# Optimization experiments

Measured on AMD Instinct MI355X. Metric: run time of the kernel, lower is better.

The kernel has to match this reference:

```python
import jax, jax.numpy as jnp
import numpy as np
from jax import lax

B, T, D, H, L, V = 4, 512, 768, 768, 2, 50257


def setup_inputs() -> dict:
    key = jax.random.key(0)
    ks = jax.random.split(key, 4)
    std = 0.02
    return {
        "reps": jax.random.normal(ks[0], (B, T, D), dtype=jnp.float32),
        "W_ih": jax.random.normal(ks[1], (L, 4 * H, D), dtype=jnp.float32) * std,
        "W_hh": jax.random.normal(ks[2], (L, 4 * H, H), dtype=jnp.float32) * std,
        "b": jnp.zeros((L, 4 * H), dtype=jnp.float32),
        "head_w": jax.random.normal(ks[3], (V, H), dtype=jnp.float32) * std,
        "head_b": jnp.zeros((V,), dtype=jnp.float32),
    }


def _lstm_layer(x_tbd, W_i, W_h, bias):
    # x_tbd: (T, B, in); returns (T, B, H) hidden sequence
    b_sz = x_tbd.shape[1]
    h_dim = W_h.shape[1]
    # precompute input projections for all timesteps: (T, B, 4H)
    xg = jnp.einsum('tbd,gd->tbg', x_tbd, W_i) + bias

    def step(carry, xt_g):
        h, c = carry
        gates = xt_g + h @ W_h.T  # (B, 4H)
        i, f, g, o = jnp.split(gates, 4, axis=-1)
        i = jax.nn.sigmoid(i)
        f = jax.nn.sigmoid(f)
        g = jnp.tanh(g)
        o = jax.nn.sigmoid(o)
        c2 = f * c + i * g
        h2 = o * jnp.tanh(c2)
        return (h2, c2), h2

    h0 = jnp.zeros((b_sz, h_dim), dtype=x_tbd.dtype)
    c0 = jnp.zeros((b_sz, h_dim), dtype=x_tbd.dtype)
    _, ys = lax.scan(step, (h0, c0), xg)
    return ys


def reference(reps, W_ih, W_hh, b, head_w, head_b):
    # reps: (B, T, D) -> logits (B, T, V)
    x = jnp.swapaxes(reps, 0, 1)  # (T, B, D)
    n_layers = W_ih.shape[0]
    for l in range(n_layers):
        x = _lstm_layer(x, W_ih[l], W_hh[l], b[l])
    hidden = jnp.swapaxes(x, 0, 1)  # (B, T, H)
    return jnp.einsum('bth,vh->btv', hidden, head_w) + head_b
```

## Files before the change

kernel.cpp:

```cpp
#include <hip/hip_runtime.h>
#include <hip/hip_fp16.h>
#include <cstdint>

#define B_SZ 4
#define T_SZ 512
#define D_SZ 768
#define H_SZ 768
#define G4   3072
#define V_SZ 50257
#define V_PAD 50304
#define M_SZ 2048
#define FUSE_WGS 192

using half8 = __attribute__((ext_vector_type(8))) _Float16;
using f32x4 = __attribute__((ext_vector_type(4))) float;
typedef unsigned long long ull;


__global__ void conv_A0(const float* __restrict__ reps, _Float16* __restrict__ A0) {
  int idx = blockIdx.x * blockDim.x + threadIdx.x;
  const int total = M_SZ * D_SZ;
  for (; idx < total; idx += gridDim.x * blockDim.x) {
    int k = idx % D_SZ, m = idx / D_SZ;
    int t = m >> 2, b = m & 3;
    A0[idx] = (_Float16)reps[(b * T_SZ + t) * D_SZ + k];
  }
}

__global__ void conv_cast(const float* __restrict__ src, _Float16* __restrict__ dst, int n) {
  int idx = blockIdx.x * blockDim.x + threadIdx.x;
  for (; idx < n; idx += gridDim.x * blockDim.x) dst[idx] = (_Float16)src[idx];
}

__global__ void conv_head(const float* __restrict__ w, _Float16* __restrict__ dst) {
  int idx = blockIdx.x * blockDim.x + threadIdx.x;
  const int total = V_PAD * H_SZ;
  for (; idx < total; idx += gridDim.x * blockDim.x) {
    int n = idx / H_SZ, k = idx % H_SZ;
    dst[idx] = (n < V_SZ) ? (_Float16)w[n * H_SZ + k] : (_Float16)0.f;
  }
}


__global__ __launch_bounds__(256) void gemm_bt_f16(
    const _Float16* __restrict__ A, const _Float16* __restrict__ B,
    const float* __restrict__ bias, float* __restrict__ C,
    int M, int N, int K, int mode, int Nreal)
{
  __shared__ __align__(16) _Float16 As[128][32];
  __shared__ __align__(16) _Float16 Bs[128][32];
  const int t = threadIdx.x;
  const int lane = t & 63, w = t >> 6;
  const int wr = w >> 1, wc = w & 1;
  const int m0 = blockIdx.x * 128, n0 = blockIdx.y * 128;

  f32x4 acc[4][4] = {};

  const int srow = t >> 2;
  const int scol = (t & 3) * 8;

  for (int k0 = 0; k0 < K; k0 += 32) {
    uint4 av0 = *(const uint4*)&A[(size_t)(m0 + srow) * K + k0 + scol];
    uint4 av1 = *(const uint4*)&A[(size_t)(m0 + 64 + srow) * K + k0 + scol];
    uint4 bv0 = *(const uint4*)&B[(size_t)(n0 + srow) * K + k0 + scol];
    uint4 bv1 = *(const uint4*)&B[(size_t)(n0 + 64 + srow) * K + k0 + scol];
    __syncthreads();
    *(uint4*)&As[srow][scol]      = av0;
    *(uint4*)&As[64 + srow][scol] = av1;
    *(uint4*)&Bs[srow][scol]      = bv0;
    *(uint4*)&Bs[64 + srow][scol] = bv1;
    __syncthreads();

    const int fr = lane & 15, k8 = (lane >> 4) * 8;
    half8 af[4], bf[4];
#pragma unroll
    for (int i = 0; i < 4; ++i) {
      af[i] = *(const half8*)&As[wr * 64 + i * 16 + fr][k8];
      bf[i] = *(const half8*)&Bs[wc * 64 + i * 16 + fr][k8];
    }
#pragma unroll
    for (int i = 0; i < 4; ++i)
#pragma unroll
      for (int j = 0; j < 4; ++j)
        acc[i][j] = __builtin_amdgcn_mfma_f32_16x16x32_f16(af[i], bf[j], acc[i][j], 0, 0, 0);
  }

  const int fr = lane & 15, rq = lane >> 4;
#pragma unroll
  for (int i = 0; i < 4; ++i) {
#pragma unroll
    for (int j = 0; j < 4; ++j) {
      int n = n0 + wc * 64 + j * 16 + fr;
      if (n >= Nreal) continue;
      float bv = bias[n];
#pragma unroll
      for (int r = 0; r < 4; ++r) {
        int m = m0 + wr * 64 + i * 16 + rq * 4 + r;
        float v = acc[i][j][r] + bv;
        if (mode == 0) {
          C[(size_t)m * N + n] = v;
        } else {
          int tt = m >> 2, bb = m & 3;
          C[(size_t)(bb * T_SZ + tt) * V_SZ + n] = v;
        }
      }
    }
  }
}


__global__ __launch_bounds__(256) void lstm_fused(
    const float* __restrict__ xg0,
    const float* __restrict__ Wih1,
    const float* __restrict__ Whh,
    const float* __restrict__ bias,
    ull* __restrict__ hx0p,
    ull* __restrict__ hx1p,
    _Float16* __restrict__ h1hist,
    unsigned* __restrict__ flags)
{
  __shared__ __align__(16) float h0buf[H_SZ * 4];
  __shared__ __align__(16) float h1buf[H_SZ * 4];
  __shared__ __align__(16) float red[4][8][4][4];
  __shared__ float actv[4][8][4];
  __shared__ float cst[8][4];

  const int t = threadIdx.x, lane = t & 63, wv = t >> 6;
  const bool L1 = blockIdx.x >= 96;
  const int lid = L1 ? (blockIdx.x - 96) : blockIdx.x;
  const int j0 = lid * 8;

  const float* WhhL = Whh + (L1 ? (size_t)G4 * H_SZ : 0);

  float wreg[8][12];
#pragma unroll
  for (int c = 0; c < 8; ++c)
#pragma unroll
    for (int kk = 0; kk < 12; ++kk)
      wreg[c][kk] = WhhL[(size_t)(wv * H_SZ + j0 + c) * H_SZ + kk * 64 + lane];

  float wreg2[8][12];
  if (L1) {
#pragma unroll
    for (int c = 0; c < 8; ++c)
#pragma unroll
      for (int kk = 0; kk < 12; ++kk)
        wreg2[c][kk] = Wih1[(size_t)(wv * H_SZ + j0 + c) * H_SZ + kk * 64 + lane];
  }

  const int g_ = t >> 5, c_ = (t >> 2) & 7, b_ = t & 3;

  float breg = 0.f;
  if (L1 && t < 128) breg = bias[G4 + g_ * H_SZ + j0 + c_];

  if (t < 32) cst[t >> 2][t & 3] = 0.f;

  const int elim = L1 ? 513 : 512;
  for (int e = 0; e < elim; ++e) {
    float xgv = 0.f;
    if (!L1 && t < 128)
      xgv = xg0[(size_t)((e << 2) + b_) * G4 + g_ * H_SZ + j0 + c_];

    const unsigned need = (unsigned)e;

    {
      const ull* s0 = hx0p + (size_t)(((unsigned)(e + 3)) & 3u) * 3072;
      ull v[12];
#pragma unroll
      for (int i = 0; i < 12; ++i)
        v[i] = __hip_atomic_load(&s0[t + i * 256], __ATOMIC_RELAXED, __HIP_MEMORY_SCOPE_AGENT);
      for (;;) {
        bool stale = false;
#pragma unroll
        for (int i = 0; i < 12; ++i) stale |= ((unsigned)(v[i] >> 32) < need);
        if (!stale) break;
        __builtin_amdgcn_s_sleep(1);
#pragma unroll
        for (int i = 0; i < 12; ++i)
          if ((unsigned)(v[i] >> 32) < need)
            v[i] = __hip_atomic_load(&s0[t + i * 256], __ATOMIC_RELAXED, __HIP_MEMORY_SCOPE_AGENT);
      }
#pragma unroll
      for (int i = 0; i < 12; ++i) h0buf[t + i * 256] = __uint_as_float((unsigned)v[i]);
    }
    if (L1) {
      const ull* s1 = hx1p + (size_t)(e & 1) * 3072;
      ull v[12];
#pragma unroll
      for (int i = 0; i < 12; ++i)
        v[i] = __hip_atomic_load(&s1[t + i * 256], __ATOMIC_RELAXED, __HIP_MEMORY_SCOPE_AGENT);
      for (;;) {
        bool stale = false;
#pragma unroll
        for (int i = 0; i < 12; ++i) stale |= ((unsigned)(v[i] >> 32) < need);
        if (!stale) break;
        __builtin_amdgcn_s_sleep(1);
#pragma unroll
        for (int i = 0; i < 12; ++i)
          if ((unsigned)(v[i] >> 32) < need)
            v[i] = __hip_atomic_load(&s1[t + i * 256], __ATOMIC_RELAXED, __HIP_MEMORY_SCOPE_AGENT);
      }
#pragma unroll
      for (int i = 0; i < 12; ++i) h1buf[t + i * 256] = __uint_as_float((unsigned)v[i]);
    }
    __syncthreads();

    const bool act = !L1 || (e >= 1);

    if (act) {
      float4 acc[8];
#pragma unroll
      for (int c = 0; c < 8; ++c) acc[c] = make_float4(0.f, 0.f, 0.f, 0.f);

      if (!L1) {
#pragma unroll
        for (int kk = 0; kk < 12; ++kk) {
          float4 h4 = *(const float4*)&h0buf[(kk * 64 + lane) * 4];
#pragma unroll
          for (int c = 0; c < 8; ++c) {
            float wf = wreg[c][kk];
            acc[c].x = fmaf(wf, h4.x, acc[c].x);
            acc[c].y = fmaf(wf, h4.y, acc[c].y);
            acc[c].z = fmaf(wf, h4.z, acc[c].z);
            acc[c].w = fmaf(wf, h4.w, acc[c].w);
          }
        }
      } else {
#pragma unroll
        for (int kk = 0; kk < 12; ++kk) {
          float4 x4 = *(const float4*)&h0buf[(kk * 64 + lane) * 4];
          float4 h4 = *(const float4*)&h1buf[(kk * 64 + lane) * 4];
#pragma unroll
          for (int c = 0; c < 8; ++c) {
            float wx = wreg2[c][kk], wh = wreg[c][kk];
            acc[c].x = fmaf(wx, x4.x, fmaf(wh, h4.x, acc[c].x));
            acc[c].y = fmaf(wx, x4.y, fmaf(wh, h4.y, acc[c].y));
            acc[c].z = fmaf(wx, x4.z, fmaf(wh, h4.z, acc[c].z));
            acc[c].w = fmaf(wx, x4.w, fmaf(wh, h4.w, acc[c].w));
          }
        }
      }

#pragma unroll
      for (int mask = 1; mask <= 8; mask <<= 1) {
#pragma unroll
        for (int c = 0; c < 8; ++c) {
          acc[c].x += __shfl_xor(acc[c].x, mask, 64);
          acc[c].y += __shfl_xor(acc[c].y, mask, 64);
          acc[c].z += __shfl_xor(acc[c].z, mask, 64);
          acc[c].w += __shfl_xor(acc[c].w, mask, 64);
        }
      }
      if ((lane & 15) == 0) {
        int q = lane >> 4;
#pragma unroll
        for (int c = 0; c < 8; ++c) *(float4*)&red[wv][c][q][0] = acc[c];
      }
    }
    __syncthreads();

    if (act && t < 128) {
      float s = red[g_][c_][0][b_] + red[g_][c_][1][b_] + red[g_][c_][2][b_] + red[g_][c_][3][b_]
              + (L1 ? breg : xgv);
      actv[g_][c_][b_] = (g_ == 2) ? tanhf(s) : (1.f / (1.f + expf(-s)));
    } else if (e >= 1 && t >= 128 && t < 128 + 96) {
      const int idx = 96 + (t - 128);
      const unsigned thr = L1 ? (unsigned)(e + 1) : (unsigned)(e - 1);
      while (__hip_atomic_load(&flags[idx * 32], __ATOMIC_RELAXED, __HIP_MEMORY_SCOPE_AGENT) < thr)
        __builtin_amdgcn_s_sleep(1);
    }
    __syncthreads();

    float hn_save = 0.f;
    if (t < 32) {
      if (act) {
        int c = t >> 2, b = t & 3;
        float iv = actv[0][c][b], fv = actv[1][c][b], gv = actv[2][c][b], ov = actv[3][c][b];
        float cn = fv * cst[c][b] + iv * gv;
        cst[c][b] = cn;
        float hn = ov * tanhf(cn);
        hn_save = hn;
        ull p = ((ull)(unsigned)(e + 1) << 32) | (ull)__float_as_uint(hn);
        ull* dst = L1 ? (hx1p + (size_t)((e + 1) & 1) * 3072)
                      : (hx0p + (size_t)(e & 3) * 3072);
        __hip_atomic_store(&dst[(j0 + c) * 4 + b], p,
                           __ATOMIC_RELAXED, __HIP_MEMORY_SCOPE_AGENT);
      } else if (L1) {
        int c = t >> 2, b = t & 3;
        ull p = ((ull)1u << 32);
        __hip_atomic_store(&hx1p[3072 + (j0 + c) * 4 + b], p,
                           __ATOMIC_RELAXED, __HIP_MEMORY_SCOPE_AGENT);
      }
    }

    if (wv == 0) {
      asm volatile("s_waitcnt vmcnt(0)" ::: "memory");
      if (t == 0)
        __hip_atomic_store(&flags[blockIdx.x * 32], (unsigned)(e + 2),
                           __ATOMIC_RELAXED, __HIP_MEMORY_SCOPE_AGENT);
    }

    if (L1 && act && t < 32) {
      int c = t >> 2, b = t & 3;
      h1hist[(size_t)(((e - 1) << 2) + b) * H_SZ + j0 + c] = (_Float16)hn_save;
    }
  }
}


extern "C" void kernel_launch(void* const* d_in, const int* in_sizes, int n_in,
                              void* d_out, int out_size, void* d_ws, size_t ws_size,
                              hipStream_t stream) {
  const float* reps   = (const float*)d_in[0];
  const float* W_ih   = (const float*)d_in[1];
  const float* W_hh   = (const float*)d_in[2];
  const float* bias   = (const float*)d_in[3];
  const float* head_w = (const float*)d_in[4];
  const float* head_b = (const float*)d_in[5];
  float* out = (float*)d_out;

  char* ws = (char*)d_ws;
  _Float16* A0h    = (_Float16*)(ws + 0);
  _Float16* Wih_h  = (_Float16*)(ws + 3145728);
  _Float16* Whead  = (_Float16*)(ws + 12582912);
  float*    xg0    = (float*)   (ws + 89849856);
  _Float16* h1hist = (_Float16*)(ws + 115015680);
  ull*      hx0p   = (ull*)     (ws + 118161408);
  ull*      hx1p   = (ull*)     (ws + 118259712);
  unsigned* flags  = (unsigned*)(ws + 118308864);

  hipLaunchKernelGGL(conv_A0,   dim3(1024), dim3(256), 0, stream, reps, A0h);
  hipLaunchKernelGGL(conv_cast, dim3(1024), dim3(256), 0, stream, W_ih, Wih_h, G4 * D_SZ);
  hipLaunchKernelGGL(conv_head, dim3(4096), dim3(256), 0, stream, head_w, Whead);

  hipLaunchKernelGGL(gemm_bt_f16, dim3(16, 24), dim3(256), 0, stream,
                     A0h, Wih_h, bias, xg0, M_SZ, G4, H_SZ, 0, G4);

  hipMemsetAsync(hx0p, 0, 172032, stream);
  hipLaunchKernelGGL(lstm_fused, dim3(FUSE_WGS), dim3(256), 0, stream,
                     xg0, W_ih + (size_t)G4 * D_SZ, W_hh, bias,
                     hx0p, hx1p, h1hist, flags);

  hipLaunchKernelGGL(gemm_bt_f16, dim3(16, 393), dim3(256), 0, stream,
                     h1hist, Whead, head_b, out, M_SZ, V_PAD, H_SZ, 1, V_SZ);
}
```

Before: 3.194 ms.

## Replace per-step flag barrier with 8-deep versioned ring buffers

```diff
diff --git a/kernel.cpp b/kernel.cpp
--- a/kernel.cpp
+++ b/kernel.cpp
@@ -116,11 +116,10 @@
     const float* __restrict__ bias,
     ull* __restrict__ hx0p,
     ull* __restrict__ hx1p,
-    _Float16* __restrict__ h1hist,
-    unsigned* __restrict__ flags)
+    _Float16* __restrict__ h1hist)
 {
-  __shared__ __align__(16) float h0buf[H_SZ * 4];
-  __shared__ __align__(16) float h1buf[H_SZ * 4];
+  __shared__ __align__(16) float h0buf[G4];
+  __shared__ __align__(16) float h1buf[G4];
   __shared__ __align__(16) float red[4][8][4][4];
   __shared__ float actv[4][8][4];
   __shared__ float cst[8][4];
@@ -157,14 +156,30 @@
 
   const int elim = L1 ? 513 : 512;
   for (int e = 0; e < elim; ++e) {
+    if (L1 && e == 0) {
+      if (t < 32) {
+        int c = t >> 2, b = t & 3;
+        __hip_atomic_store(&hx1p[(size_t)(j0 + c) * 4 + b], (ull)1u << 32,
+                           __ATOMIC_RELAXED, __HIP_MEMORY_SCOPE_AGENT);
+      }
+      continue;
+    }
+
     float xgv = 0.f;
     if (!L1 && t < 128)
       xgv = xg0[(size_t)((e << 2) + b_) * G4 + g_ * H_SZ + j0 + c_];
 
+    if (!L1 && t == 0 && e >= 5) {
+      const ull* bp = hx1p + (size_t)((e - 5) & 7) * G4;
+      while ((unsigned)(__hip_atomic_load(bp, __ATOMIC_RELAXED, __HIP_MEMORY_SCOPE_AGENT) >> 32)
+             < (unsigned)(e - 4))
+        __builtin_amdgcn_s_sleep(1);
+    }
+
     const unsigned need = (unsigned)e;
 
     {
-      const ull* s0 = hx0p + (size_t)(((unsigned)(e + 3)) & 3u) * 3072;
+      const ull* s0 = hx0p + (size_t)((e + 7) & 7) * G4;
       ull v[12];
 #pragma unroll
       for (int i = 0; i < 12; ++i)
@@ -184,7 +199,7 @@
       for (int i = 0; i < 12; ++i) h0buf[t + i * 256] = __uint_as_float((unsigned)v[i]);
     }
     if (L1) {
-      const ull* s1 = hx1p + (size_t)(e & 1) * 3072;
+      const ull* s1 = hx1p + (size_t)((e + 7) & 7) * G4;
       ull v[12];
 #pragma unroll
       for (int i = 0; i < 12; ++i)
@@ -205,104 +220,75 @@
     }
     __syncthreads();
 
-    const bool act = !L1 || (e >= 1);
-
-    if (act) {
-      float4 acc[8];
-#pragma unroll
-      for (int c = 0; c < 8; ++c) acc[c] = make_float4(0.f, 0.f, 0.f, 0.f);
-
-      if (!L1) {
-#pragma unroll
-        for (int kk = 0; kk < 12; ++kk) {
-          float4 h4 = *(const float4*)&h0buf[(kk * 64 + lane) * 4];
-#pragma unroll
-          for (int c = 0; c < 8; ++c) {
-            float wf = wreg[c][kk];
-            acc[c].x = fmaf(wf, h4.x, acc[c].x);
-            acc[c].y = fmaf(wf, h4.y, acc[c].y);
-            acc[c].z = fmaf(wf, h4.z, acc[c].z);
-            acc[c].w = fmaf(wf, h4.w, acc[c].w);
-          }
+    float4 acc[8];
+#pragma unroll
+    for (int c = 0; c < 8; ++c) acc[c] = make_float4(0.f, 0.f, 0.f, 0.f);
+
+    if (!L1) {
+#pragma unroll
+      for (int kk = 0; kk < 12; ++kk) {
+        float4 h4 = *(const float4*)&h0buf[(kk * 64 + lane) * 4];
+#pragma unroll
+        for (int c = 0; c < 8; ++c) {
+          float wf = wreg[c][kk];
+          acc[c].x = fmaf(wf, h4.x, acc[c].x);
+          acc[c].y = fmaf(wf, h4.y, acc[c].y);
+          acc[c].z = fmaf(wf, h4.z, acc[c].z);
+          acc[c].w = fmaf(wf, h4.w, acc[c].w);
         }
-      } else {
-#pragma unroll
-        for (int kk = 0; kk < 12; ++kk) {
-          float4 x4 = *(const float4*)&h0buf[(kk * 64 + lane) * 4];
-          float4 h4 = *(const float4*)&h1buf[(kk * 64 + lane) * 4];
-#pragma unroll
-          for (int c = 0; c < 8; ++c) {
-            float wx = wreg2[c][kk], wh = wreg[c][kk];
-            acc[c].x = fmaf(wx, x4.x, fmaf(wh, h4.x, acc[c].x));
-            acc[c].y = fmaf(wx, x4.y, fmaf(wh, h4.y, acc[c].y));
-            acc[c].z = fmaf(wx, x4.z, fmaf(wh, h4.z, acc[c].z));
-            acc[c].w = fmaf(wx, x4.w, fmaf(wh, h4.w, acc[c].w));
-          }
+      }
+    } else {
+#pragma unroll
+      for (int kk = 0; kk < 12; ++kk) {
+        float4 x4 = *(const float4*)&h0buf[(kk * 64 + lane) * 4];
+        float4 h4 = *(const float4*)&h1buf[(kk * 64 + lane) * 4];
+#pragma unroll
+        for (int c = 0; c < 8; ++c) {
+          float wx = wreg2[c][kk], wh = wreg[c][kk];
+          acc[c].x = fmaf(wx, x4.x, fmaf(wh, h4.x, acc[c].x));
+          acc[c].y = fmaf(wx, x4.y, fmaf(wh, h4.y, acc[c].y));
+          acc[c].z = fmaf(wx, x4.z, fmaf(wh, h4.z, acc[c].z));
+          acc[c].w = fmaf(wx, x4.w, fmaf(wh, h4.w, acc[c].w));
         }
       }
-
-#pragma unroll
-      for (int mask = 1; mask <= 8; mask <<= 1) {
-#pragma unroll
-        for (int c = 0; c < 8; ++c) {
-          acc[c].x += __shfl_xor(acc[c].x, mask, 64);
-          acc[c].y += __shfl_xor(acc[c].y, mask, 64);
-          acc[c].z += __shfl_xor(acc[c].z, mask, 64);
-          acc[c].w += __shfl_xor(acc[c].w, mask, 64);
-        }
-      }
-      if ((lane & 15) == 0) {
-        int q = lane >> 4;
-#pragma unroll
-        for (int c = 0; c < 8; ++c) *(float4*)&red[wv][c][q][0] = acc[c];
-      }
-    }
-    __syncthreads();
-
-    if (act && t < 128) {
+    }
+
+#pragma unroll
+    for (int mask = 1; mask <= 8; mask <<= 1) {
+#pragma unroll
+      for (int c = 0; c < 8; ++c) {
+        acc[c].x += __shfl_xor(acc[c].x, mask, 64);
+        acc[c].y += __shfl_xor(acc[c].y, mask, 64);
+        acc[c].z += __shfl_xor(acc[c].z, mask, 64);
+        acc[c].w += __shfl_xor(acc[c].w, mask, 64);
+      }
+    }
+    if ((lane & 15) == 0) {
+      int q = lane >> 4;
+#pragma unroll
+      for (int c = 0; c < 8; ++c) *(float4*)&red[wv][c][q][0] = acc[c];
+    }
+    __syncthreads();
+
+    if (t < 128) {
       float s = red[g_][c_][0][b_] + red[g_][c_][1][b_] + red[g_][c_][2][b_] + red[g_][c_][3][b_]
               + (L1 ? breg : xgv);
       actv[g_][c_][b_] = (g_ == 2) ? tanhf(s) : (1.f / (1.f + expf(-s)));
-    } else if (e >= 1 && t >= 128 && t < 128 + 96) {
-      const int idx = 96 + (t - 128);
-      const unsigned thr = L1 ? (unsigned)(e + 1) : (unsigned)(e - 1);
-      while (__hip_atomic_load(&flags[idx * 32], __ATOMIC_RELAXED, __HIP_MEMORY_SCOPE_AGENT) < thr)
-        __builtin_amdgcn_s_sleep(1);
-    }
-    __syncthreads();
-
-    float hn_save = 0.f;
+    }
+    __syncthreads();
+
     if (t < 32) {
-      if (act) {
-        int c = t >> 2, b = t & 3;
-        float iv = actv[0][c][b], fv = actv[1][c][b], gv = actv[2][c][b], ov = actv[3][c][b];
-        float cn = fv * cst[c][b] + iv * gv;
-        cst[c][b] = cn;
-        float hn = ov * tanhf(cn);
-        hn_save = hn;
-        ull p = ((ull)(unsigned)(e + 1) << 32) | (ull)__float_as_uint(hn);
-        ull* dst = L1 ? (hx1p + (size_t)((e + 1) & 1) * 3072)
-                      : (hx0p + (size_t)(e & 3) * 3072);
-        __hip_atomic_store(&dst[(j0 + c) * 4 + b], p,
-                           __ATOMIC_RELAXED, __HIP_MEMORY_SCOPE_AGENT);
-      } else if (L1) {
-        int c = t >> 2, b = t & 3;
-        ull p = ((ull)1u << 32);
-        __hip_atomic_store(&hx1p[3072 + (j0 + c) * 4 + b], p,
-                           __ATOMIC_RELAXED, __HIP_MEMORY_SCOPE_AGENT);
-      }
-    }
-
-    if (wv == 0) {
-      asm volatile("s_waitcnt vmcnt(0)" ::: "memory");
-      if (t == 0)
-        __hip_atomic_store(&flags[blockIdx.x * 32], (unsigned)(e + 2),
-                           __ATOMIC_RELAXED, __HIP_MEMORY_SCOPE_AGENT);
-    }
-
-    if (L1 && act && t < 32) {
       int c = t >> 2, b = t & 3;
-      h1hist[(size_t)(((e - 1) << 2) + b) * H_SZ + j0 + c] = (_Float16)hn_save;
+      float iv = actv[0][c][b], fv = actv[1][c][b], gv = actv[2][c][b], ov = actv[3][c][b];
+      float cn = fv * cst[c][b] + iv * gv;
+      cst[c][b] = cn;
+      float hn = ov * tanhf(cn);
+      ull p = ((ull)(unsigned)(e + 1) << 32) | (ull)__float_as_uint(hn);
+      ull* dst = (L1 ? hx1p : hx0p) + (size_t)(e & 7) * G4;
+      __hip_atomic_store(&dst[(size_t)(j0 + c) * 4 + b], p,
+                         __ATOMIC_RELAXED, __HIP_MEMORY_SCOPE_AGENT);
+      if (L1)
+        h1hist[(size_t)(((e - 1) << 2) + b) * H_SZ + j0 + c] = (_Float16)hn;
     }
   }
 }
@@ -326,8 +312,7 @@
   float*    xg0    = (float*)   (ws + 89849856);
   _Float16* h1hist = (_Float16*)(ws + 115015680);
   ull*      hx0p   = (ull*)     (ws + 118161408);
-  ull*      hx1p   = (ull*)     (ws + 118259712);
-  unsigned* flags  = (unsigned*)(ws + 118308864);
+  ull*      hx1p   = (ull*)     (ws + 118358016);
 
   hipLaunchKernelGGL(conv_A0,   dim3(1024), dim3(256), 0, stream, reps, A0h);
   hipLaunchKernelGGL(conv_cast, dim3(1024), dim3(256), 0, stream, W_ih, Wih_h, G4 * D_SZ);
@@ -336,10 +321,10 @@
   hipLaunchKernelGGL(gemm_bt_f16, dim3(16, 24), dim3(256), 0, stream,
                      A0h, Wih_h, bias, xg0, M_SZ, G4, H_SZ, 0, G4);
 
-  hipMemsetAsync(hx0p, 0, 172032, stream);
+  hipMemsetAsync(hx0p, 0, 393216, stream);
   hipLaunchKernelGGL(lstm_fused, dim3(FUSE_WGS), dim3(256), 0, stream,
                      xg0, W_ih + (size_t)G4 * D_SZ, W_hh, bias,
-                     hx0p, hx1p, h1hist, flags);
+                     hx0p, hx1p, h1hist);
 
   hipLaunchKernelGGL(gemm_bt_f16, dim3(16, 393), dim3(256), 0, stream,
                      h1hist, Whead, head_b, out, M_SZ, V_PAD, H_SZ, 1, V_SZ);
```

New measurement: 3.017 ms. 5.5% less time.
